# Performance work log

Hardware: AMD Instinct MI355X
Metric: run time of the kernel (lower is better)

## Reference

```python
import jax, jax.numpy as jnp
import numpy as np
from jax import lax

B, N, FD, D, H, LH, HC, NC = 8, 1024, 34, 64, 4, 128, 193, 9
STEPS, ET = 4, 2
DH = D // H
LHH = LH // 2  # hidden per LSTM direction
SCALE = float(1.0 / np.sqrt(DH))
BN_INV = float(1.0 / np.sqrt(1.0 + 1e-5))  # BatchNorm eval with running var=1


def layernorm(x, g, b, eps=1e-5):
    m = x.mean(-1, keepdims=True)
    v = ((x - m) ** 2).mean(-1, keepdims=True)
    return (x - m) / jnp.sqrt(v + eps) * g + b


def mha(q_in, kv, w, b, ow, ob):
    # torch nn.MultiheadAttention, batch_first, eval (no dropout)
    wq, wk, wv = jnp.split(w, 3, 0)
    bq, bk, bv = jnp.split(b, 3, 0)
    q = (q_in @ wq.T + bq).reshape(B, N, H, DH)
    k = (kv @ wk.T + bk).reshape(B, N, H, DH)
    v = (kv @ wv.T + bv).reshape(B, N, H, DH)
    s = jnp.einsum('bqhd,bkhd->bhqk', q, k) * SCALE
    a = jax.nn.softmax(s, -1)
    o = jnp.einsum('bhqk,bkhd->bqhd', a, v).reshape(B, N, D)
    return o @ ow.T + ob


def gru(x, h, wih, whh, bih, bhh):
    gi = x @ wih.T + bih
    gh = h @ whh.T + bhh
    ir, iz, inn = jnp.split(gi, 3, -1)
    hr, hz, hn = jnp.split(gh, 3, -1)
    r = jax.nn.sigmoid(ir + hr)
    z = jax.nn.sigmoid(iz + hz)
    n = jnp.tanh(inn + r * hn)
    return (1.0 - z) * n + z * h


def lstm_dir(x, wih, whh, b, reverse):
    hd = wih.shape[0] // 4
    def step(carry, xt):
        h, c = carry
        g = xt @ wih.T + h @ whh.T + b
        i, f, gg, o = jnp.split(g, 4, -1)
        c = jax.nn.sigmoid(f) * c + jax.nn.sigmoid(i) * jnp.tanh(gg)
        h = jax.nn.sigmoid(o) * jnp.tanh(c)
        return (h, c), h
    xs = jnp.swapaxes(x, 0, 1)
    if reverse:
        xs = xs[::-1]
    z0 = jnp.zeros((x.shape[0], hd), x.dtype)
    (hf, _), hs = lax.scan(step, (z0, z0), xs)
    if reverse:
        hs = hs[::-1]
    return jnp.swapaxes(hs, 0, 1), hf


def forward(node_features, adj_data, adj_control, handcrafted_features,
            ip_w, ip_b, et_w, mha_in_w, mha_in_b, mha_out_w, mha_out_b,
            eta_w1, eta_b1, eta_w2, eta_b2, gru_wih, gru_whh, gru_bih, gru_bhh,
            ln_g, ln_b, oln_g, oln_b,
            l0f_wih, l0f_whh, l0f_b, l0b_wih, l0b_whh, l0b_b,
            l1f_wih, l1f_whh, l1f_b, l1b_wih, l1b_whh, l1b_b,
            attn_w1, attn_b1, attn_w2, attn_b2,
            hc_w1, hc_b1, bn1_g, bn1_b, hc_w2, hc_b2, bn2_g, bn2_b, hc_w3, hc_b3,
            cls_w1, cls_b1, cls_w2, cls_b2, cls_w3, cls_b3,
            topo_order, node_mask, seq_lengths):
    # input projection
    h = jax.nn.relu(node_features @ ip_w.T + ip_b)
    adjs = (adj_data, adj_control)
    for l in range(STEPS):
        msgs = []
        for e in range(ET):
            ht = h @ et_w[l, e].T
            m = mha(h, ht, mha_in_w[l, e], mha_in_b[l, e], mha_out_w[l, e], mha_out_b[l, e])
            msgs.append(jnp.einsum('bij,bjd->bid', adjs[e], m))
        st = jnp.stack(msgs, 2)            # [B,N,ET,D]
        ctx = st.mean(2)
        ai = jnp.concatenate([h, ctx], -1)
        etw = jax.nn.softmax(jax.nn.relu(ai @ eta_w1[l].T + eta_b1[l]) @ eta_w2[l].T + eta_b2[l], -1)
        messages = (st * etw[..., None]).sum(2)
        hn = gru(messages, h, gru_wih[l], gru_whh[l], gru_bih[l], gru_bhh[l])
        hn = layernorm(hn, ln_g[l], ln_b[l])
        h = layernorm(h + hn, oln_g[l], oln_b[l])
    h = h * node_mask.astype(h.dtype)[..., None]
    h_ord = jnp.take_along_axis(h, topo_order[..., None], 1)
    # 2-layer BiLSTM
    o0f, _ = lstm_dir(h_ord, l0f_wih, l0f_whh, l0f_b, False)
    o0b, _ = lstm_dir(h_ord, l0b_wih, l0b_whh, l0b_b, True)
    o0 = jnp.concatenate([o0f, o0b], -1)
    o1f, h1f = lstm_dir(o0, l1f_wih, l1f_whh, l1f_b, False)
    o1b, h1b = lstm_dir(o0, l1b_wih, l1b_whh, l1b_b, True)
    h_all = jnp.concatenate([o1f, o1b], -1)    # [B,N,LH]
    final = jnp.concatenate([h1f, h1b], -1)    # [B,LH]
    # masked attention pooling
    scores = (jnp.tanh(h_all @ attn_w1.T + attn_b1) @ attn_w2.T + attn_b2)[..., 0]
    smask = jnp.arange(N)[None, :] < seq_lengths[:, None]
    aw = jax.nn.softmax(jnp.where(smask, scores, -1e9), -1)
    pooled = jnp.einsum('bt,btd->bd', aw, h_all)
    comb = pooled + final
    # handcrafted encoder (BN in eval mode, running stats 0/1)
    x = jax.nn.relu(handcrafted_features @ hc_w1.T + hc_b1)
    x = x * BN_INV * bn1_g + bn1_b
    x = jax.nn.relu(x @ hc_w2.T + hc_b2)
    x = x * BN_INV * bn2_g + bn2_b
    x = jax.nn.relu(x @ hc_w3.T + hc_b3)
    hf = jnp.concatenate([comb, x], -1)
    y = jax.nn.relu(hf @ cls_w1.T + cls_b1)
    y = jax.nn.relu(y @ cls_w2.T + cls_b2)
    return y @ cls_w3.T + cls_b3


def setup_inputs():
    key = jax.random.key(0)
    ks = iter(jax.random.split(key, 128))
    def rn(shape, s=0.05):
        return (jax.random.normal(next(ks), shape) * s).astype(jnp.float32)
    inp = {}
    inp['node_features'] = jax.random.normal(next(ks), (B, N, FD), jnp.float32)
    inp['adj_data'] = jax.random.uniform(next(ks), (B, N, N), jnp.float32) * (2.0 / N)
    inp['adj_control'] = jax.random.uniform(next(ks), (B, N, N), jnp.float32) * (2.0 / N)
    inp['handcrafted_features'] = jax.random.normal(next(ks), (B, HC), jnp.float32)
    inp['ip_w'] = rn((D, FD)); inp['ip_b'] = rn((D,))
    inp['et_w'] = rn((STEPS, ET, D, D))
    inp['mha_in_w'] = rn((STEPS, ET, 3 * D, D)); inp['mha_in_b'] = rn((STEPS, ET, 3 * D))
    inp['mha_out_w'] = rn((STEPS, ET, D, D)); inp['mha_out_b'] = rn((STEPS, ET, D))
    inp['eta_w1'] = rn((STEPS, D, 2 * D)); inp['eta_b1'] = rn((STEPS, D))
    inp['eta_w2'] = rn((STEPS, ET, D)); inp['eta_b2'] = rn((STEPS, ET))
    inp['gru_wih'] = rn((STEPS, 3 * D, D)); inp['gru_whh'] = rn((STEPS, 3 * D, D))
    inp['gru_bih'] = rn((STEPS, 3 * D)); inp['gru_bhh'] = rn((STEPS, 3 * D))
    inp['ln_g'] = jnp.ones((STEPS, D), jnp.float32); inp['ln_b'] = jnp.zeros((STEPS, D), jnp.float32)
    inp['oln_g'] = jnp.ones((STEPS, D), jnp.float32); inp['oln_b'] = jnp.zeros((STEPS, D), jnp.float32)
    inp['l0f_wih'] = rn((4 * LHH, D)); inp['l0f_whh'] = rn((4 * LHH, LHH)); inp['l0f_b'] = rn((4 * LHH,))
    inp['l0b_wih'] = rn((4 * LHH, D)); inp['l0b_whh'] = rn((4 * LHH, LHH)); inp['l0b_b'] = rn((4 * LHH,))
    inp['l1f_wih'] = rn((4 * LHH, LH)); inp['l1f_whh'] = rn((4 * LHH, LHH)); inp['l1f_b'] = rn((4 * LHH,))
    inp['l1b_wih'] = rn((4 * LHH, LH)); inp['l1b_whh'] = rn((4 * LHH, LHH)); inp['l1b_b'] = rn((4 * LHH,))
    inp['attn_w1'] = rn((64, LH)); inp['attn_b1'] = rn((64,))
    inp['attn_w2'] = rn((1, 64)); inp['attn_b2'] = rn((1,))
    inp['hc_w1'] = rn((256, HC)); inp['hc_b1'] = rn((256,))
    inp['bn1_g'] = jnp.ones((256,), jnp.float32); inp['bn1_b'] = jnp.zeros((256,), jnp.float32)
    inp['hc_w2'] = rn((128, 256)); inp['hc_b2'] = rn((128,))
    inp['bn2_g'] = jnp.ones((128,), jnp.float32); inp['bn2_b'] = jnp.zeros((128,), jnp.float32)
    inp['hc_w3'] = rn((64, 128)); inp['hc_b3'] = rn((64,))
    inp['cls_w1'] = rn((128, LH + 64)); inp['cls_b1'] = rn((128,))
    inp['cls_w2'] = rn((64, 128)); inp['cls_b2'] = rn((64,))
    inp['cls_w3'] = rn((NC, 64)); inp['cls_b3'] = rn((NC,))
    inp['topo_order'] = jax.vmap(lambda k: jax.random.permutation(k, N))(jax.random.split(next(ks), B))
    inp['node_mask'] = jnp.ones((B, N), bool)
    inp['seq_lengths'] = jax.random.randint(next(ks), (B,), N // 2, N + 1)
    return inp


def reference(node_features, adj_data, adj_control, handcrafted_features,
              ip_w, ip_b, et_w, mha_in_w, mha_in_b, mha_out_w, mha_out_b,
              eta_w1, eta_b1, eta_w2, eta_b2, gru_wih, gru_whh, gru_bih, gru_bhh,
              ln_g, ln_b, oln_g, oln_b,
              l0f_wih, l0f_whh, l0f_b, l0b_wih, l0b_whh, l0b_b,
              l1f_wih, l1f_whh, l1f_b, l1b_wih, l1b_whh, l1b_b,
              attn_w1, attn_b1, attn_w2, attn_b2,
              hc_w1, hc_b1, bn1_g, bn1_b, hc_w2, hc_b2, bn2_g, bn2_b, hc_w3, hc_b3,
              cls_w1, cls_b1, cls_w2, cls_b2, cls_w3, cls_b3,
              topo_order, node_mask, seq_lengths):
    return forward(node_features, adj_data, adj_control, handcrafted_features,
                   ip_w, ip_b, et_w, mha_in_w, mha_in_b, mha_out_w, mha_out_b,
                   eta_w1, eta_b1, eta_w2, eta_b2, gru_wih, gru_whh, gru_bih, gru_bhh,
                   ln_g, ln_b, oln_g, oln_b,
                   l0f_wih, l0f_whh, l0f_b, l0b_wih, l0b_whh, l0b_b,
                   l1f_wih, l1f_whh, l1f_b, l1b_wih, l1b_whh, l1b_b,
                   attn_w1, attn_b1, attn_w2, attn_b2,
                   hc_w1, hc_b1, bn1_g, bn1_b, hc_w2, hc_b2, bn2_g, bn2_b, hc_w3, hc_b3,
                   cls_w1, cls_b1, cls_w2, cls_b2, cls_w3, cls_b3,
                   topo_order, node_mask, seq_lengths)
```

## Files before the change

kernel.cpp:

```cpp
#include <hip/hip_runtime.h>
#include <math.h>

#define NB 8
#define NN 1024
#define NT 8192
#define SCALE_C 0.25f
#define BN_INV_C 0.99999500003749969f
#define LN_EPS 1e-5f

typedef __attribute__((ext_vector_type(8))) short bf16x8;
typedef __attribute__((ext_vector_type(4))) float f32x4;

__device__ __forceinline__ float sigmoidf_(float x){ return 1.f/(1.f+__expf(-x)); }
__device__ __forceinline__ float tanhf_(float x){
  float ax = fabsf(x);
  float e = __expf(-2.f*ax);
  float t = (1.f-e)/(1.f+e);
  return x < 0.f ? -t : t;
}
__device__ __forceinline__ float wsum64(float v){
  #pragma unroll
  for (int m=1; m<64; m<<=1) v += __shfl_xor(v, m);
  return v;
}
__device__ __forceinline__ unsigned short f2bf(float f){
  unsigned int u = __float_as_uint(f);
  unsigned int r = (u + 0x7fffu + ((u>>16)&1u)) >> 16;
  return (unsigned short)r;
}

__global__ __launch_bounds__(256) void gemm_tn(
    const float* __restrict__ A, long aZ,
    const float* __restrict__ W, long wZ,
    const float* __restrict__ Bias, long bZ,
    float* __restrict__ C, long cZ,
    int M, int Ncols, int K, int act)
{
  const int z = blockIdx.z;
  A += (long)z * aZ; W += (long)z * wZ; C += (long)z * cZ;
  if (Bias) Bias += (long)z * bZ;
  const int m0 = blockIdx.x * 64;
  const int n0 = blockIdx.y * 64;
  const int tid = threadIdx.x;
  __shared__ float As[16][68];
  __shared__ float Ws[16][68];
  const int lm = tid >> 2;
  const int kq = (tid & 3) * 4;
  const int tr = tid >> 4;
  const int tc = tid & 15;
  float acc[4][4] = {};
  const bool v16 = ((K & 15) == 0);
  for (int kt = 0; kt < K; kt += 16) {
    if (v16) {
      float4 a = *reinterpret_cast<const float4*>(&A[(long)(m0 + lm) * K + kt + kq]);
      As[kq+0][lm]=a.x; As[kq+1][lm]=a.y; As[kq+2][lm]=a.z; As[kq+3][lm]=a.w;
      float4 w = *reinterpret_cast<const float4*>(&W[(long)(n0 + lm) * K + kt + kq]);
      Ws[kq+0][lm]=w.x; Ws[kq+1][lm]=w.y; Ws[kq+2][lm]=w.z; Ws[kq+3][lm]=w.w;
    } else {
      #pragma unroll
      for (int j = 0; j < 4; ++j) {
        int k = kt + kq + j;
        As[kq+j][lm] = (k < K) ? A[(long)(m0+lm)*K + k] : 0.f;
        Ws[kq+j][lm] = (k < K) ? W[(long)(n0+lm)*K + k] : 0.f;
      }
    }
    __syncthreads();
    #pragma unroll
    for (int k = 0; k < 16; ++k) {
      float4 av = *reinterpret_cast<const float4*>(&As[k][tr*4]);
      float4 wv = *reinterpret_cast<const float4*>(&Ws[k][tc*4]);
      float a_[4] = {av.x,av.y,av.z,av.w};
      float w_[4] = {wv.x,wv.y,wv.z,wv.w};
      #pragma unroll
      for (int i=0;i<4;++i)
        #pragma unroll
        for (int j=0;j<4;++j) acc[i][j] += a_[i]*w_[j];
    }
    __syncthreads();
  }
  #pragma unroll
  for (int i=0;i<4;++i) {
    const long m = m0 + tr*4 + i;
    #pragma unroll
    for (int j=0;j<4;++j) {
      const int n = n0 + tc*4 + j;
      float v = acc[i][j];
      if (Bias) v += Bias[n];
      if (act) v = fmaxf(v, 0.f);
      C[m*Ncols + n] = v;
    }
  }
}

__global__ __launch_bounds__(256) void wprep(
    const float* __restrict__ miw, const float* __restrict__ etw,
    float* __restrict__ wcomb)
{
  const int le = blockIdx.x;
  const float* Wm = miw + (long)le*192*64;
  const float* Et = etw + (long)le*64*64;
  float* Out = wcomb + (long)le*192*64;
  __shared__ float es[64][65];
  const int tid = threadIdx.x;
  for (int i = tid; i < 4096; i += 256) es[i>>6][i&63] = Et[i];
  __syncthreads();
  for (int i = tid; i < 4096; i += 256) Out[i] = Wm[i];
  for (int i = tid; i < 8192; i += 256) {
    const int r = 64 + (i >> 6), d = i & 63;
    const float* wr = &Wm[(long)r*64];
    float a = 0.f;
    #pragma unroll 8
    for (int c = 0; c < 64; ++c) a += wr[c] * es[c][d];
    Out[(long)r*64 + d] = a;
  }
}

__global__ __launch_bounds__(256) void mcvt_kernel(
    const float* __restrict__ m0, const float* __restrict__ m1,
    unsigned short* __restrict__ mmT)
{
  const int e = blockIdx.y;
  const float* src = e ? m1 : m0;
  unsigned short* dst = mmT + (long)e*64*8192;
  const int r0 = blockIdx.x * 64;
  __shared__ unsigned short tile[64][65];
  const int tid = threadIdx.x;
  const int lr = tid >> 2, c0 = (tid & 3) * 16;
  #pragma unroll
  for (int i = 0; i < 16; i += 4) {
    float4 v = *reinterpret_cast<const float4*>(&src[(long)(r0+lr)*64 + c0 + i]);
    tile[lr][c0+i+0] = f2bf(v.x);
    tile[lr][c0+i+1] = f2bf(v.y);
    tile[lr][c0+i+2] = f2bf(v.z);
    tile[lr][c0+i+3] = f2bf(v.w);
  }
  __syncthreads();
  const int n = tid >> 2, rr = (tid & 3) * 16;
  #pragma unroll
  for (int i = 0; i < 16; i += 4) {
    ushort4 w;
    w.x = tile[rr+i+0][n];
    w.y = tile[rr+i+1][n];
    w.z = tile[rr+i+2][n];
    w.w = tile[rr+i+3][n];
    *reinterpret_cast<ushort4*>(&dst[(long)n*8192 + r0 + rr + i]) = w;
  }
}

__global__ __launch_bounds__(256) void gemm_nn_mfma(
    const float* __restrict__ adjD, const float* __restrict__ adjC,
    const unsigned short* __restrict__ mmT,
    float* __restrict__ msg)
{
  const int z = blockIdx.z;
  const int e = z >> 3, b = z & 7;
  const float* A = (e ? adjC : adjD) + (long)b*NN*NN;
  const unsigned short* Bt = mmT + (long)e*64*8192 + (long)b*NN;
  float* Cp = msg + ((long)e*NT + (long)b*NN) * 64;
  const int tid = threadIdx.x;
  const int w = tid >> 6;
  const int l = tid & 63;
  const int r = l & 15;
  const int kg = l >> 4;
  const long arow = (long)(blockIdx.x*64 + w*16 + r) * NN;

  f32x4 acc0 = {0.f,0.f,0.f,0.f}, acc1 = acc0, acc2 = acc0, acc3 = acc0;

  for (int k0 = 0; k0 < NN; k0 += 32) {
    const float4* ap = reinterpret_cast<const float4*>(&A[arow + k0 + kg*8]);
    float4 a0 = ap[0], a1 = ap[1];
    union { unsigned short us[8]; bf16x8 v; } au;
    au.us[0]=f2bf(a0.x); au.us[1]=f2bf(a0.y); au.us[2]=f2bf(a0.z); au.us[3]=f2bf(a0.w);
    au.us[4]=f2bf(a1.x); au.us[5]=f2bf(a1.y); au.us[6]=f2bf(a1.z); au.us[7]=f2bf(a1.w);
    bf16x8 b0 = *reinterpret_cast<const bf16x8*>(&Bt[(long)(0*16+r)*8192 + k0 + kg*8]);
    bf16x8 b1 = *reinterpret_cast<const bf16x8*>(&Bt[(long)(1*16+r)*8192 + k0 + kg*8]);
    bf16x8 b2 = *reinterpret_cast<const bf16x8*>(&Bt[(long)(2*16+r)*8192 + k0 + kg*8]);
    bf16x8 b3 = *reinterpret_cast<const bf16x8*>(&Bt[(long)(3*16+r)*8192 + k0 + kg*8]);
    acc0 = __builtin_amdgcn_mfma_f32_16x16x32_bf16(au.v, b0, acc0, 0, 0, 0);
    acc1 = __builtin_amdgcn_mfma_f32_16x16x32_bf16(au.v, b1, acc1, 0, 0, 0);
    acc2 = __builtin_amdgcn_mfma_f32_16x16x32_bf16(au.v, b2, acc2, 0, 0, 0);
    acc3 = __builtin_amdgcn_mfma_f32_16x16x32_bf16(au.v, b3, acc3, 0, 0, 0);
  }
  const int crow = blockIdx.x*64 + w*16 + kg*4;
  #pragma unroll
  for (int i = 0; i < 4; ++i) {
    Cp[(long)(crow+i)*64 + 0*16 + r] = acc0[i];
    Cp[(long)(crow+i)*64 + 1*16 + r] = acc1[i];
    Cp[(long)(crow+i)*64 + 2*16 + r] = acc2[i];
    Cp[(long)(crow+i)*64 + 3*16 + r] = acc3[i];
  }
}

__global__ __launch_bounds__(256) void attn_kernel(
    const float* __restrict__ qkv, float* __restrict__ O)
{
  const int e = blockIdx.z;
  const float* base = qkv + (long)e*1572864;
  float* o = O + (long)e*524288;
  const int bh = blockIdx.y;
  const int b = bh >> 2, head = bh & 3;
  const int q0 = blockIdx.x * 64;
  const int tid = threadIdx.x;
  const int r = tid >> 2, p = tid & 3;
  const long row = (long)b*NN + q0 + r;
  float qreg[16];
  {
    const float4* qp = reinterpret_cast<const float4*>(&base[row*192 + head*16]);
    #pragma unroll
    for (int i=0;i<4;++i) {
      float4 v = qp[i];
      qreg[4*i+0]=v.x*SCALE_C; qreg[4*i+1]=v.y*SCALE_C;
      qreg[4*i+2]=v.z*SCALE_C; qreg[4*i+3]=v.w*SCALE_C;
    }
  }
  float mx = -1e30f, ssum = 0.f, acc[16];
  #pragma unroll
  for (int d=0;d<16;++d) acc[d]=0.f;
  __shared__ float ks[128][17];
  __shared__ float vs[128][17];
  for (int j0 = 0; j0 < NN; j0 += 128) {
    {
      const int jr = tid >> 1;
      const int hf = (tid & 1) * 8;
      const long rr = ((long)b*NN + j0 + jr)*192 + head*16 + hf;
      const float4* kp = reinterpret_cast<const float4*>(&base[rr + 64]);
      float4 k0 = kp[0], k1 = kp[1];
      ks[jr][hf+0]=k0.x; ks[jr][hf+1]=k0.y; ks[jr][hf+2]=k0.z; ks[jr][hf+3]=k0.w;
      ks[jr][hf+4]=k1.x; ks[jr][hf+5]=k1.y; ks[jr][hf+6]=k1.z; ks[jr][hf+7]=k1.w;
      const float4* vp = reinterpret_cast<const float4*>(&base[rr + 128]);
      float4 v0 = vp[0], v1 = vp[1];
      vs[jr][hf+0]=v0.x; vs[jr][hf+1]=v0.y; vs[jr][hf+2]=v0.z; vs[jr][hf+3]=v0.w;
      vs[jr][hf+4]=v1.x; vs[jr][hf+5]=v1.y; vs[jr][hf+6]=v1.z; vs[jr][hf+7]=v1.w;
    }
    __syncthreads();
    for (int jj = p; jj < 128; jj += 4) {
      float s = 0.f;
      #pragma unroll
      for (int d=0;d<16;++d) s += qreg[d]*ks[jj][d];
      if (s <= mx) {
        float ee = __expf(s - mx);
        ssum += ee;
        #pragma unroll
        for (int d=0;d<16;++d) acc[d] += ee*vs[jj][d];
      } else {
        float cc = __expf(mx - s);
        ssum = ssum*cc + 1.f;
        #pragma unroll
        for (int d=0;d<16;++d) acc[d] = acc[d]*cc + vs[jj][d];
        mx = s;
      }
    }
    __syncthreads();
  }
  #pragma unroll
  for (int mask=1; mask<=2; mask<<=1) {
    float om = __shfl_xor(mx, mask);
    float os = __shfl_xor(ssum, mask);
    float nm = fmaxf(mx, om);
    float c1 = __expf(mx-nm), c2 = __expf(om-nm);
    ssum = ssum*c1 + os*c2;
    #pragma unroll
    for (int d=0;d<16;++d) {
      float ov = __shfl_xor(acc[d], mask);
      acc[d] = acc[d]*c1 + ov*c2;
    }
    mx = nm;
  }
  if (p == 0) {
    float inv = 1.f/ssum;
    float4* op = reinterpret_cast<float4*>(&o[row*64 + head*16]);
    #pragma unroll
    for (int i=0;i<4;++i) {
      float4 v;
      v.x=acc[4*i+0]*inv; v.y=acc[4*i+1]*inv; v.z=acc[4*i+2]*inv; v.w=acc[4*i+3]*inv;
      op[i] = v;
    }
  }
}

__global__ __launch_bounds__(64) void fused_gate_gru_ln(
    float* __restrict__ h, const float* __restrict__ msg0, const float* __restrict__ msg1,
    const float* __restrict__ ew1, const float* __restrict__ eb1,
    const float* __restrict__ ew2, const float* __restrict__ eb2,
    const float* __restrict__ wih, const float* __restrict__ whh,
    const float* __restrict__ bih, const float* __restrict__ bhh,
    const float* __restrict__ lng, const float* __restrict__ lnb,
    const float* __restrict__ olng, const float* __restrict__ olnb)
{
  const int r0 = blockIdx.x * 4;
  const int tid = threadIdx.x;
  __shared__ float hsm[4][64], m0s[4][64], m1s[4][64], tss[4][64];
  #pragma unroll
  for (int r=0;r<4;++r) {
    hsm[r][tid] = h[(long)(r0+r)*64 + tid];
    m0s[r][tid] = msg0[(long)(r0+r)*64 + tid];
    m1s[r][tid] = msg1[(long)(r0+r)*64 + tid];
  }
  __syncthreads();
  float ta[4] = {0.f,0.f,0.f,0.f};
  for (int k=0;k<64;++k) {
    float w = ew1[tid*128 + k];
    #pragma unroll
    for (int r=0;r<4;++r) ta[r] += w * hsm[r][k];
  }
  for (int k=0;k<64;++k) {
    float w = ew1[tid*128 + 64 + k];
    #pragma unroll
    for (int r=0;r<4;++r) ta[r] += w * 0.5f*(m0s[r][k]+m1s[r][k]);
  }
  #pragma unroll
  for (int r=0;r<4;++r) tss[r][tid] = fmaxf(ta[r] + eb1[tid], 0.f);
  __syncthreads();
  const float w2a = ew2[tid], w2b = ew2[64+tid];
  #pragma unroll
  for (int r=0;r<4;++r) {
    float l0 = wsum64(tss[r][tid]*w2a) + eb2[0];
    float l1 = wsum64(tss[r][tid]*w2b) + eb2[1];
    float mm = fmaxf(l0,l1);
    float e0 = __expf(l0-mm), e1 = __expf(l1-mm);
    float wgt0 = e0/(e0+e1);
    m0s[r][tid] = wgt0*m0s[r][tid] + (1.f-wgt0)*m1s[r][tid];
  }
  __syncthreads();
  float air[4]={},aiz[4]={},ain[4]={},ahr[4]={},ahz[4]={},ahn[4]={};
  for (int k=0;k<64;++k) {
    float wir = wih[(long)tid*64 + k];
    float wiz = wih[(long)(64+tid)*64 + k];
    float win = wih[(long)(128+tid)*64 + k];
    float whr = whh[(long)tid*64 + k];
    float whz = whh[(long)(64+tid)*64 + k];
    float whn = whh[(long)(128+tid)*64 + k];
    #pragma unroll
    for (int r=0;r<4;++r) {
      float x = m0s[r][k], hh = hsm[r][k];
      air[r] += wir*x; aiz[r] += wiz*x; ain[r] += win*x;
      ahr[r] += whr*hh; ahz[r] += whz*hh; ahn[r] += whn*hh;
    }
  }
  const float bir = bih[tid], biz = bih[64+tid], bin_ = bih[128+tid];
  const float bhr = bhh[tid], bhz = bhh[64+tid], bhn = bhh[128+tid];
  const float g1 = lng[tid], b1v = lnb[tid], g2 = olng[tid], b2v = olnb[tid];
  #pragma unroll
  for (int r=0;r<4;++r) {
    float rg = sigmoidf_(air[r]+bir + ahr[r]+bhr);
    float zg = sigmoidf_(aiz[r]+biz + ahz[r]+bhz);
    float ng = tanhf_(ain[r]+bin_ + rg*(ahn[r]+bhn));
    float hnv = (1.f-zg)*ng + zg*hsm[r][tid];
    float mu = wsum64(hnv) * 0.015625f;
    float dv = hnv - mu;
    float var = wsum64(dv*dv) * 0.015625f;
    float y = dv * rsqrtf(var + LN_EPS) * g1 + b1v;
    float ho = hsm[r][tid] + y;
    float mu2 = wsum64(ho) * 0.015625f;
    float d2 = ho - mu2;
    float var2 = wsum64(d2*d2) * 0.015625f;
    h[(long)(r0+r)*64 + tid] = d2 * rsqrtf(var2 + LN_EPS) * g2 + b2v;
  }
}

__global__ __launch_bounds__(256) void permute_kernel(
    const float* __restrict__ h, const int* __restrict__ topo, float* __restrict__ ho)
{
  const long idx = (long)blockIdx.x*256 + threadIdx.x;
  const int row = (int)(idx >> 6), d = (int)(idx & 63);
  const int b = row >> 10, i = row & 1023;
  const int src = topo[b*1024 + i];
  ho[idx] = h[((long)b*1024 + src)*64 + d];
}

__global__ __launch_bounds__(256, 1) void lstm_seq(
    const float* __restrict__ xpF, const float* __restrict__ xpB,
    const float* __restrict__ whhF, const float* __restrict__ whhB,
    float* __restrict__ out)
{
  const int b = blockIdx.x;
  const int dir = blockIdx.y;
  const float* xp = dir ? xpB : xpF;
  const float* W  = dir ? whhB : whhF;
  const int colOff = dir * 64;
  const int tid = threadIdx.x;
  const int wv  = tid >> 6;
  const int j   = tid & 63;

  float4 wreg[16];
  {
    const float4* wp = reinterpret_cast<const float4*>(&W[tid*64]);
    #pragma unroll
    for (int i=0;i<16;++i) wreg[i] = wp[i];
  }

  __shared__ __align__(16) float hs[2][64];
  __shared__ float g5[2][320];
  __shared__ __align__(16) float ring[16][256];
  float c = 0.f;
  if (tid < 64) hs[0][tid] = 0.f;
  __syncthreads();

  const long rowb = (long)b*NN;
  #pragma unroll
  for (int s = 0; s < 8; ++s) {
    const int ts = dir ? (NN-1-s) : s;
    __builtin_amdgcn_global_load_lds(
        (const __attribute__((address_space(1))) void*)(&xp[(rowb + ts)*256 + tid]),
        (__attribute__((address_space(3))) void*)(&ring[s][wv*64]), 4, 0, 0);
  }

  int p = 0;
  for (int t = 0; t < NN; ++t) {
    const int cur = dir ? (NN-1-t) : t;
    if (t + 8 < NN) {
      asm volatile("s_waitcnt vmcnt(7)" ::: "memory");
      const int ts2 = dir ? (NN-9-t) : (t+8);
      __builtin_amdgcn_global_load_lds(
          (const __attribute__((address_space(1))) void*)(&xp[(rowb + ts2)*256 + tid]),
          (__attribute__((address_space(3))) void*)(&ring[(t+8)&15][wv*64]), 4, 0, 0);
    } else {
      asm volatile("s_waitcnt vmcnt(0)" ::: "memory");
    }
    const float x = ring[t & 15][tid];

    float a0 = x, a1 = 0.f, a2 = 0.f, a3 = 0.f;
    #pragma unroll
    for (int k=0;k<16;k+=4) {
      float4 h0 = *reinterpret_cast<const float4*>(&hs[p][k*4]);
      float4 h1 = *reinterpret_cast<const float4*>(&hs[p][k*4+4]);
      float4 h2 = *reinterpret_cast<const float4*>(&hs[p][k*4+8]);
      float4 h3 = *reinterpret_cast<const float4*>(&hs[p][k*4+12]);
      a0 += wreg[k].x*h0.x + wreg[k].y*h0.y + wreg[k].z*h0.z + wreg[k].w*h0.w;
      a1 += wreg[k+1].x*h1.x + wreg[k+1].y*h1.y + wreg[k+1].z*h1.z + wreg[k+1].w*h1.w;
      a2 += wreg[k+2].x*h2.x + wreg[k+2].y*h2.y + wreg[k+2].z*h2.z + wreg[k+2].w*h2.w;
      a3 += wreg[k+3].x*h3.x + wreg[k+3].y*h3.y + wreg[k+3].z*h3.z + wreg[k+3].w*h3.w;
    }
    float dot = (a0+a1)+(a2+a3);
    float v = (wv == 2) ? tanhf_(dot) : sigmoidf_(dot);
    g5[p][j*5 + wv] = v;
    asm volatile("s_waitcnt lgkmcnt(0)" ::: "memory");
    __builtin_amdgcn_s_barrier();
    const float gi = g5[p][j*5+0];
    const float gf = g5[p][j*5+1];
    const float gg = g5[p][j*5+2];
    const float go = g5[p][j*5+3];
    c = gf*c + gi*gg;
    const float hval = go * tanhf_(c);
    hs[p^1][j] = hval;
    if (tid < 64) out[(rowb + cur)*128 + colOff + j] = hval;
    p ^= 1;
  }
}

__global__ __launch_bounds__(64) void score_kernel(
    const float* __restrict__ h_all, const float* __restrict__ w1,
    const float* __restrict__ b1, const float* __restrict__ w2,
    const float* __restrict__ b2, float* __restrict__ scores)
{
  const int row = blockIdx.x, tid = threadIdx.x;
  __shared__ float xs[128];
  xs[tid]    = h_all[(long)row*128 + tid];
  xs[64+tid] = h_all[(long)row*128 + 64 + tid];
  __syncthreads();
  float a = b1[tid];
  for (int k=0;k<128;++k) a += w1[tid*128+k]*xs[k];
  float s = tanhf_(a) * w2[tid];
  s = wsum64(s);
  if (tid==0) scores[row] = s + b2[0];
}

__global__ __launch_bounds__(256) void pool_kernel(
    const float* __restrict__ h_all, const float* __restrict__ scores,
    const int* __restrict__ seqlen, float* __restrict__ comb)
{
  const int b = blockIdx.x, tid = threadIdx.x;
  __shared__ float aw[1024];
  __shared__ float red[4];
  __shared__ float part[256];
  const int L = seqlen[b];
  float mx = -1e30f;
  for (int t = tid; t < 1024; t += 256) {
    float s = (t < L) ? scores[b*1024+t] : -1e30f;
    aw[t] = s;
    mx = fmaxf(mx, s);
  }
  #pragma unroll
  for (int m=1;m<64;m<<=1) mx = fmaxf(mx, __shfl_xor(mx,m));
  if ((tid&63)==0) red[tid>>6] = mx;
  __syncthreads();
  mx = fmaxf(fmaxf(red[0],red[1]), fmaxf(red[2],red[3]));
  __syncthreads();
  float ss = 0.f;
  for (int t = tid; t < 1024; t += 256) {
    float e = (t < L) ? __expf(aw[t]-mx) : 0.f;
    aw[t] = e; ss += e;
  }
  ss = wsum64(ss);
  if ((tid&63)==0) red[tid>>6] = ss;
  __syncthreads();
  ss = red[0]+red[1]+red[2]+red[3];
  const float inv = 1.f/ss;
  const int d = tid & 127, hseg = tid >> 7;
  float acc = 0.f;
  for (int t = hseg; t < 1024; t += 2)
    acc += aw[t] * h_all[((long)b*1024 + t)*128 + d];
  part[tid] = acc;
  __syncthreads();
  if (tid < 128) {
    float pooled = (part[tid] + part[tid+128]) * inv;
    float fin = (tid < 64) ? h_all[((long)b*1024 + 1023)*128 + tid]
                           : h_all[((long)b*1024 + 0)*128 + tid];
    comb[b*128 + tid] = pooled + fin;
  }
}

__global__ __launch_bounds__(256) void head_kernel(
    const float* __restrict__ comb, const float* __restrict__ hcf,
    const float* __restrict__ w1, const float* __restrict__ b1,
    const float* __restrict__ bn1g, const float* __restrict__ bn1b,
    const float* __restrict__ w2, const float* __restrict__ b2,
    const float* __restrict__ bn2g, const float* __restrict__ bn2b,
    const float* __restrict__ w3, const float* __restrict__ b3,
    const float* __restrict__ cw1, const float* __restrict__ cb1,
    const float* __restrict__ cw2, const float* __restrict__ cb2,
    const float* __restrict__ cw3, const float* __restrict__ cb3,
    float* __restrict__ outp)
{
  const int b = blockIdx.x, tid = threadIdx.x;
  __shared__ float hrow[193];
  __shared__ float x1[256], x2[128], hf[192], y1[128], y2[64];
  if (tid < 193) hrow[tid] = hcf[b*193 + tid];
  if (tid < 128) hf[tid] = comb[b*128 + tid];
  __syncthreads();
  {
    float a = b1[tid];
    for (int k=0;k<193;++k) a += w1[(long)tid*193+k]*hrow[k];
    x1[tid] = fmaxf(a,0.f)*BN_INV_C*bn1g[tid] + bn1b[tid];
  }
  __syncthreads();
  if (tid < 128) {
    float a = b2[tid];
    for (int k=0;k<256;++k) a += w2[(long)tid*256+k]*x1[k];
    x2[tid] = fmaxf(a,0.f)*BN_INV_C*bn2g[tid] + bn2b[tid];
  }
  __syncthreads();
  if (tid < 64) {
    float a = b3[tid];
    for (int k=0;k<128;++k) a += w3[(long)tid*128+k]*x2[k];
    hf[128+tid] = fmaxf(a,0.f);
  }
  __syncthreads();
  if (tid < 128) {
    float a = cb1[tid];
    for (int k=0;k<192;++k) a += cw1[(long)tid*192+k]*hf[k];
    y1[tid] = fmaxf(a,0.f);
  }
  __syncthreads();
  if (tid < 64) {
    float a = cb2[tid];
    for (int k=0;k<128;++k) a += cw2[(long)tid*128+k]*y1[k];
    y2[tid] = fmaxf(a,0.f);
  }
  __syncthreads();
  if (tid < 9) {
    float a = cb3[tid];
    for (int k=0;k<64;++k) a += cw3[(long)tid*64+k]*y2[k];
    outp[b*9+tid] = a;
  }
}

extern "C" void kernel_launch(void* const* d_in, const int* in_sizes, int n_in,
                              void* d_out, int out_size, void* d_ws, size_t ws_size,
                              hipStream_t stream)
{
  const float* nf   = (const float*)d_in[0];
  const float* adjD = (const float*)d_in[1];
  const float* adjC = (const float*)d_in[2];
  const float* hcf  = (const float*)d_in[3];
  const float* ip_w = (const float*)d_in[4];
  const float* ip_b = (const float*)d_in[5];
  const float* et_w = (const float*)d_in[6];
  const float* miw  = (const float*)d_in[7];
  const float* mib  = (const float*)d_in[8];
  const float* mow  = (const float*)d_in[9];
  const float* mob  = (const float*)d_in[10];
  const float* ew1  = (const float*)d_in[11];
  const float* eb1  = (const float*)d_in[12];
  const float* ew2  = (const float*)d_in[13];
  const float* eb2  = (const float*)d_in[14];
  const float* gwih = (const float*)d_in[15];
  const float* gwhh = (const float*)d_in[16];
  const float* gbih = (const float*)d_in[17];
  const float* gbhh = (const float*)d_in[18];
  const float* lng  = (const float*)d_in[19];
  const float* lnb  = (const float*)d_in[20];
  const float* olng = (const float*)d_in[21];
  const float* olnb = (const float*)d_in[22];
  const float* l0f_wih = (const float*)d_in[23];
  const float* l0f_whh = (const float*)d_in[24];
  const float* l0f_b   = (const float*)d_in[25];
  const float* l0b_wih = (const float*)d_in[26];
  const float* l0b_whh = (const float*)d_in[27];
  const float* l0b_b   = (const float*)d_in[28];
  const float* l1f_wih = (const float*)d_in[29];
  const float* l1f_whh = (const float*)d_in[30];
  const float* l1f_b   = (const float*)d_in[31];
  const float* l1b_wih = (const float*)d_in[32];
  const float* l1b_whh = (const float*)d_in[33];
  const float* l1b_b   = (const float*)d_in[34];
  const float* aw1  = (const float*)d_in[35];
  const float* ab1  = (const float*)d_in[36];
  const float* aw2  = (const float*)d_in[37];
  const float* ab2  = (const float*)d_in[38];
  const float* hw1  = (const float*)d_in[39];
  const float* hb1  = (const float*)d_in[40];
  const float* bn1g = (const float*)d_in[41];
  const float* bn1b = (const float*)d_in[42];
  const float* hw2  = (const float*)d_in[43];
  const float* hb2  = (const float*)d_in[44];
  const float* bn2g = (const float*)d_in[45];
  const float* bn2b = (const float*)d_in[46];
  const float* hw3  = (const float*)d_in[47];
  const float* hb3  = (const float*)d_in[48];
  const float* cw1  = (const float*)d_in[49];
  const float* cb1  = (const float*)d_in[50];
  const float* cw2  = (const float*)d_in[51];
  const float* cb2  = (const float*)d_in[52];
  const float* cw3  = (const float*)d_in[53];
  const float* cb3  = (const float*)d_in[54];
  const int*  topo  = (const int*)d_in[55];
  const int*  seqlen= (const int*)d_in[57];

  float* ws = (float*)d_ws;
  float* h     = ws;
  float* qkv   = ws + 524288;
  float* ob    = ws + 3670016;
  float* mbuf  = ws + 4718592;
  float* msg   = ws + 5767168;
  unsigned short* mmT = (unsigned short*)(ws + 6815744);
  float* wcomb = ws + 7340032;
  float* hord  = ws + 524288;
  float* xpf   = ws + 1048576;
  float* xpb   = ws + 3145728;
  float* o0    = ws + 5767168;
  float* hall  = ws + 7438336;
  float* sc    = ws + 8486912;
  float* comb  = ws + 8495104;

  dim3 blk(256);

  wprep<<<dim3(8), blk, 0, stream>>>(miw, et_w, wcomb);

  gemm_tn<<<dim3(128,1,1), blk, 0, stream>>>(nf,0, ip_w,0, ip_b,0, h,0, NT,64,34, 1);

  for (int l=0; l<4; ++l) {
    const float* mowl = mow + (size_t)l*2*64*64;
    const float* mobl = mob + (size_t)l*2*64;
    gemm_tn<<<dim3(128,3,2), blk, 0, stream>>>(h,0, wcomb + (size_t)l*2*12288, 12288,
                                               mib + (size_t)l*2*192, 192,
                                               qkv, 1572864, NT,192,64, 0);
    attn_kernel<<<dim3(16,32,2), blk, 0, stream>>>(qkv, ob);
    gemm_tn<<<dim3(128,1,2), blk, 0, stream>>>(ob,524288, mowl,4096, mobl,64, mbuf,524288, NT,64,64, 0);
    mcvt_kernel<<<dim3(128,2), blk, 0, stream>>>(mbuf, mbuf+524288, mmT);
    gemm_nn_mfma<<<dim3(16,1,16), blk, 0, stream>>>(adjD, adjC, mmT, msg);
    fused_gate_gru_ln<<<dim3(2048), dim3(64), 0, stream>>>(h, msg, msg+524288,
        ew1 + (size_t)l*64*128, eb1 + l*64, ew2 + l*128, eb2 + l*2,
        gwih + (size_t)l*192*64, gwhh + (size_t)l*192*64, gbih + l*192, gbhh + l*192,
        lng + l*64, lnb + l*64, olng + l*64, olnb + l*64);
  }

  permute_kernel<<<dim3(2048), blk, 0, stream>>>(h, topo, hord);

  gemm_tn<<<dim3(128,4,1), blk, 0, stream>>>(hord,0, l0f_wih,0, l0f_b,0, xpf,0, NT,256,64, 0);
  gemm_tn<<<dim3(128,4,1), blk, 0, stream>>>(hord,0, l0b_wih,0, l0b_b,0, xpb,0, NT,256,64, 0);
  lstm_seq<<<dim3(8,2), blk, 0, stream>>>(xpf, xpb, l0f_whh, l0b_whh, o0);
  gemm_tn<<<dim3(128,4,1), blk, 0, stream>>>(o0,0, l1f_wih,0, l1f_b,0, xpf,0, NT,256,128, 0);
  gemm_tn<<<dim3(128,4,1), blk, 0, stream>>>(o0,0, l1b_wih,0, l1b_b,0, xpb,0, NT,256,128, 0);
  lstm_seq<<<dim3(8,2), blk, 0, stream>>>(xpf, xpb, l1f_whh, l1b_whh, hall);

  score_kernel<<<dim3(8192), dim3(64), 0, stream>>>(hall, aw1, ab1, aw2, ab2, sc);
  pool_kernel<<<dim3(8), blk, 0, stream>>>(hall, sc, seqlen, comb);
  head_kernel<<<dim3(8), blk, 0, stream>>>(comb, hcf,
      hw1,hb1,bn1g,bn1b, hw2,hb2,bn2g,bn2b, hw3,hb3,
      cw1,cb1, cw2,cb2, cw3,cb3, (float*)d_out);
}
```

Measured before the change: 3.224 ms.

## Run LSTM recurrence in a single wavefront with fp16 dot2 weights

The sequential LSTM kernel goes from four wavefronts (one per gate, exchanging gate values through shared memory with a block barrier every timestep) to one 64-thread wavefront. Each lane now computes all four gates for its hidden unit, which removes the per-step barrier and the shared-memory gate exchange. To fit 4x64x64 recurrent weights in registers, they are stored as packed fp16 and the dot products use v_dot2 fp16 instructions; the hidden state is also kept in fp16. This trades accuracy (fp16 weights and state over 1024 recurrent steps) and four-way parallelism per step for lower synchronisation latency on the critical serial path.

```diff
diff --git a/kernel.cpp b/kernel.cpp
--- a/kernel.cpp
+++ b/kernel.cpp
@@ -10,6 +10,7 @@
 
 typedef __attribute__((ext_vector_type(8))) short bf16x8;
 typedef __attribute__((ext_vector_type(4))) float f32x4;
+typedef _Float16 h2 __attribute__((ext_vector_type(2)));
 
 __device__ __forceinline__ float sigmoidf_(float x){ return 1.f/(1.f+__expf(-x)); }
 __device__ __forceinline__ float tanhf_(float x){
@@ -368,7 +369,7 @@
   ho[idx] = h[((long)b*1024 + src)*64 + d];
 }
 
-__global__ __launch_bounds__(256, 1) void lstm_seq(
+__global__ __launch_bounds__(64, 1) void lstm_seq(
     const float* __restrict__ xpF, const float* __restrict__ xpB,
     const float* __restrict__ whhF, const float* __restrict__ whhB,
     float* __restrict__ out)
@@ -378,72 +379,68 @@
   const float* xp = dir ? xpB : xpF;
   const float* W  = dir ? whhB : whhF;
   const int colOff = dir * 64;
-  const int tid = threadIdx.x;
-  const int wv  = tid >> 6;
-  const int j   = tid & 63;
-
-  float4 wreg[16];
-  {
-    const float4* wp = reinterpret_cast<const float4*>(&W[tid*64]);
-    #pragma unroll
-    for (int i=0;i<16;++i) wreg[i] = wp[i];
-  }
-
-  __shared__ __align__(16) float hs[2][64];
-  __shared__ float g5[2][320];
+  const int j = threadIdx.x;
+
+  h2 Wp[4][32];
+  #pragma unroll
+  for (int c = 0; c < 4; ++c) {
+    const float* wr = &W[(long)(c*64 + j)*64];
+    #pragma unroll
+    for (int k = 0; k < 32; ++k) {
+      h2 v; v.x = (_Float16)wr[2*k]; v.y = (_Float16)wr[2*k+1];
+      Wp[c][k] = v;
+    }
+  }
+
+  __shared__ __align__(16) _Float16 hs[2][64];
   __shared__ __align__(16) float ring[16][256];
+  hs[0][j] = (_Float16)0.f;
   float c = 0.f;
-  if (tid < 64) hs[0][tid] = 0.f;
-  __syncthreads();
+  asm volatile("s_waitcnt lgkmcnt(0)" ::: "memory");
 
   const long rowb = (long)b*NN;
   #pragma unroll
   for (int s = 0; s < 8; ++s) {
     const int ts = dir ? (NN-1-s) : s;
     __builtin_amdgcn_global_load_lds(
-        (const __attribute__((address_space(1))) void*)(&xp[(rowb + ts)*256 + tid]),
-        (__attribute__((address_space(3))) void*)(&ring[s][wv*64]), 4, 0, 0);
+        (const __attribute__((address_space(1))) void*)(&xp[(rowb + ts)*256 + j*4]),
+        (__attribute__((address_space(3))) void*)(&ring[s][j*4]), 16, 0, 0);
   }
 
   int p = 0;
   for (int t = 0; t < NN; ++t) {
     const int cur = dir ? (NN-1-t) : t;
     if (t + 8 < NN) {
-      asm volatile("s_waitcnt vmcnt(7)" ::: "memory");
+      if (t < 8) { asm volatile("s_waitcnt vmcnt(7)"  ::: "memory"); }
+      else       { asm volatile("s_waitcnt vmcnt(15)" ::: "memory"); }
       const int ts2 = dir ? (NN-9-t) : (t+8);
       __builtin_amdgcn_global_load_lds(
-          (const __attribute__((address_space(1))) void*)(&xp[(rowb + ts2)*256 + tid]),
-          (__attribute__((address_space(3))) void*)(&ring[(t+8)&15][wv*64]), 4, 0, 0);
+          (const __attribute__((address_space(1))) void*)(&xp[(rowb + ts2)*256 + j*4]),
+          (__attribute__((address_space(3))) void*)(&ring[(t+8)&15][j*4]), 16, 0, 0);
     } else {
       asm volatile("s_waitcnt vmcnt(0)" ::: "memory");
     }
-    const float x = ring[t & 15][tid];
-
-    float a0 = x, a1 = 0.f, a2 = 0.f, a3 = 0.f;
-    #pragma unroll
-    for (int k=0;k<16;k+=4) {
-      float4 h0 = *reinterpret_cast<const float4*>(&hs[p][k*4]);
-      float4 h1 = *reinterpret_cast<const float4*>(&hs[p][k*4+4]);
-      float4 h2 = *reinterpret_cast<const float4*>(&hs[p][k*4+8]);
-      float4 h3 = *reinterpret_cast<const float4*>(&hs[p][k*4+12]);
-      a0 += wreg[k].x*h0.x + wreg[k].y*h0.y + wreg[k].z*h0.z + wreg[k].w*h0.w;
-      a1 += wreg[k+1].x*h1.x + wreg[k+1].y*h1.y + wreg[k+1].z*h1.z + wreg[k+1].w*h1.w;
-      a2 += wreg[k+2].x*h2.x + wreg[k+2].y*h2.y + wreg[k+2].z*h2.z + wreg[k+2].w*h2.w;
-      a3 += wreg[k+3].x*h3.x + wreg[k+3].y*h3.y + wreg[k+3].z*h3.z + wreg[k+3].w*h3.w;
-    }
-    float dot = (a0+a1)+(a2+a3);
-    float v = (wv == 2) ? tanhf_(dot) : sigmoidf_(dot);
-    g5[p][j*5 + wv] = v;
+    const float* rs = &ring[t & 15][0];
+    float aI = rs[j], aF = rs[64+j], aG = rs[128+j], aO = rs[192+j];
+
+    const h2* hv = reinterpret_cast<const h2*>(&hs[p][0]);
+    #pragma unroll
+    for (int k = 0; k < 32; ++k) {
+      h2 hh = hv[k];
+      aI = __builtin_amdgcn_fdot2(Wp[0][k], hh, aI, false);
+      aF = __builtin_amdgcn_fdot2(Wp[1][k], hh, aF, false);
+      aG = __builtin_amdgcn_fdot2(Wp[2][k], hh, aG, false);
+      aO = __builtin_amdgcn_fdot2(Wp[3][k], hh, aO, false);
+    }
+    const float ig = sigmoidf_(aI);
+    const float fg = sigmoidf_(aF);
+    const float gg = tanhf_(aG);
+    const float og = sigmoidf_(aO);
+    c = fg*c + ig*gg;
+    const float hval = og * tanhf_(c);
+    hs[p^1][j] = (_Float16)hval;
     asm volatile("s_waitcnt lgkmcnt(0)" ::: "memory");
-    __builtin_amdgcn_s_barrier();
-    const float gi = g5[p][j*5+0];
-    const float gf = g5[p][j*5+1];
-    const float gg = g5[p][j*5+2];
-    const float go = g5[p][j*5+3];
-    c = gf*c + gi*gg;
-    const float hval = go * tanhf_(c);
-    hs[p^1][j] = hval;
-    if (tid < 64) out[(rowb + cur)*128 + colOff + j] = hval;
+    out[(rowb + cur)*128 + colOff + j] = hval;
     p ^= 1;
   }
 }
@@ -669,10 +666,10 @@
 
   gemm_tn<<<dim3(128,4,1), blk, 0, stream>>>(hord,0, l0f_wih,0, l0f_b,0, xpf,0, NT,256,64, 0);
   gemm_tn<<<dim3(128,4,1), blk, 0, stream>>>(hord,0, l0b_wih,0, l0b_b,0, xpb,0, NT,256,64, 0);
-  lstm_seq<<<dim3(8,2), blk, 0, stream>>>(xpf, xpb, l0f_whh, l0b_whh, o0);
+  lstm_seq<<<dim3(8,2), dim3(64), 0, stream>>>(xpf, xpb, l0f_whh, l0b_whh, o0);
   gemm_tn<<<dim3(128,4,1), blk, 0, stream>>>(o0,0, l1f_wih,0, l1f_b,0, xpf,0, NT,256,128, 0);
   gemm_tn<<<dim3(128,4,1), blk, 0, stream>>>(o0,0, l1b_wih,0, l1b_b,0, xpb,0, NT,256,128, 0);
-  lstm_seq<<<dim3(8,2), blk, 0, stream>>>(xpf, xpb, l1f_whh, l1b_whh, hall);
+  lstm_seq<<<dim3(8,2), dim3(64), 0, stream>>>(xpf, xpb, l1f_whh, l1b_whh, hall);
 
   score_kernel<<<dim3(8192), dim3(64), 0, stream>>>(hall, aw1, ab1, aw2, ab2, sc);
   pool_kernel<<<dim3(8), blk, 0, stream>>>(hall, sc, seqlen, comb);
```

After: 3.190 ms. Within noise of the previous version (-1.1%).
